# Optimization experiments

Measured on AMD Instinct MI355X. Metric: run time of the kernel, lower is better.

The kernel has to match this reference:

```python
import jax, jax.numpy as jnp
import numpy as np

BETA = 0.25  # commitment_beta from CodebookDecoder default


def setup_inputs() -> dict:
    key = jax.random.key(0)
    k1, k2, k3 = jax.random.split(key, 3)
    Q, B, K, D = 2048, 40000, 2048, 512
    return {
        "query_emb": jax.random.normal(k1, (Q, D), dtype=jnp.float32),
        "entity_emb": jax.random.normal(k2, (B, D), dtype=jnp.float32),
        "codebook": jax.random.normal(k3, (K, D), dtype=jnp.float32),
    }


def _quantize(x, codebook):
    # Nearest-neighbor lookup. torch.norm(x[:,None]-cb[None]) argmin is
    # equivalent to argmin of squared distance, expanded to avoid the
    x2 = jnp.sum(x * x, axis=1, keepdims=True)            # (B, 1)
    c2 = jnp.sum(codebook * codebook, axis=1)             # (K,)
    d2 = x2 - 2.0 * (x @ codebook.T) + c2[None, :]        # (B, K)
    idx = jnp.argmin(d2, axis=1)                          # (B,)
    quant = codebook[idx]                                 # (B, D) gather
    # vq_loss = mse(quant.detach(), x) + beta * mse(quant, x.detach())
    vq_loss = jnp.mean((jax.lax.stop_gradient(quant) - x) ** 2) \
        + BETA * jnp.mean((quant - jax.lax.stop_gradient(x)) ** 2)
    return quant, idx, vq_loss


def reference(query_emb, entity_emb, codebook):
    quant, idx, vq_loss = _quantize(entity_emb, codebook)
    score = query_emb @ quant.T                           # (Q, B)
    return score, vq_loss, idx
```

## Files before the change

### kernel.cpp

```cpp
#include <hip/hip_runtime.h>
#include <stdint.h>

#define Q    2048
#define NB   40000
#define NK   2048
#define ND   512
#define SCORE_SIZE (Q * NB)

#define BM 256
#define BN 256
#define BK 64

typedef __bf16 bf16;
typedef bf16  bf16x8 __attribute__((ext_vector_type(8)));
typedef float f32x4  __attribute__((ext_vector_type(4)));

__device__ __forceinline__ unsigned short f2bf_rne(float f) {
    unsigned int u = __float_as_uint(f);
    u += 0x7FFFu + ((u >> 16) & 1u);
    return (unsigned short)(u >> 16);
}

__device__ __forceinline__ void gl2lds16(const void* g, void* l) {
    __builtin_amdgcn_global_load_lds(
        (const __attribute__((address_space(1))) void*)g,
        (__attribute__((address_space(3))) void*)l, 16, 0, 0);
}

__global__ __launch_bounds__(256) void c2_kernel(const float* __restrict__ cb,
                                                 float* __restrict__ c2) {
    int wave = threadIdx.x >> 6, lane = threadIdx.x & 63;
    int row  = blockIdx.x * 4 + wave;
    const float4* p = (const float4*)(cb + (size_t)row * ND);
    float4 a = p[lane];
    float4 b = p[lane + 64];
    float s = a.x*a.x + a.y*a.y + a.z*a.z + a.w*a.w
            + b.x*b.x + b.y*b.y + b.z*b.z + b.w*b.w;
    #pragma unroll
    for (int off = 32; off; off >>= 1) s += __shfl_down(s, off);
    if (lane == 0) c2[row] = s;
}

__global__ __launch_bounds__(256) void cvt_bf16_kernel(const float* __restrict__ src,
                                                       unsigned short* __restrict__ dst) {
    int i = (blockIdx.x * 256 + threadIdx.x) * 4;
    float4 v = *(const float4*)(src + i);
    uint2 u;
    u.x = (unsigned int)f2bf_rne(v.x) | ((unsigned int)f2bf_rne(v.y) << 16);
    u.y = (unsigned int)f2bf_rne(v.z) | ((unsigned int)f2bf_rne(v.w) << 16);
    *(uint2*)(dst + i) = u;
}

__device__ __forceinline__ void top2_insert(float& v1, int& i1, float& v2, int& i2,
                                            float w, int j) {
    if (w < v1 || (w == v1 && j < i1)) { v2 = v1; i2 = i1; v1 = w; i1 = j; }
    else if (w < v2 || (w == v2 && j < i2)) { v2 = w; i2 = j; }
}

__device__ __forceinline__ void mfma_tile256(const unsigned short* __restrict__ Ab,
                                             const unsigned short* __restrict__ Bb,
                                             f32x4 (&acc)[8][4],
                                             int wm, int wn, int lr, int quad) {
    #pragma unroll
    for (int kq = 0; kq < 2; ++kq) {
        bf16x8 af[8], bfr[4];
        #pragma unroll
        for (int mi = 0; mi < 8; ++mi) {
            int r = wm * 128 + mi * 16 + lr;
            int ch = (kq * 4 + quad) ^ (lr & 7);
            af[mi] = *(const bf16x8*)(Ab + ((size_t)r * 8 + ch) * 8);
        }
        #pragma unroll
        for (int ni = 0; ni < 4; ++ni) {
            int r = wn * 64 + ni * 16 + lr;
            int ch = (kq * 4 + quad) ^ (lr & 7);
            bfr[ni] = *(const bf16x8*)(Bb + ((size_t)r * 8 + ch) * 8);
        }
        #pragma unroll
        for (int mi = 0; mi < 8; ++mi)
            #pragma unroll
            for (int ni = 0; ni < 4; ++ni)
                acc[mi][ni] = __builtin_amdgcn_mfma_f32_16x16x32_bf16(
                    af[mi], bfr[ni], acc[mi][ni], 0, 0, 0);
    }
}

__device__ __forceinline__ void tile_coords8(int bid, int& fast8, int& slow157) {
    int wg = (bid & 7) * 157 + (bid >> 3);
    fast8   = wg & 7;
    slow157 = wg >> 3;
}

template<bool PRE>
__device__ __forceinline__ void stage_dist256(
        const float* __restrict__ entf, const unsigned short* __restrict__ ehi,
        const unsigned short* __restrict__ chi,
        unsigned short* Eb, unsigned short* Cb,
        int b0, int k0, int kt, int tid, int wave) {
    #pragma unroll
    for (int j = 0; j < 4; ++j) {
        int q = j * 512 + tid;
        int r = q >> 3;
        int cs = (q & 7) ^ (r & 7);
        gl2lds16(chi + (size_t)(k0 + r) * ND + kt + cs * 8,
                 Cb + (size_t)(j * 512 + wave * 64) * 8);
        int br = b0 + r; br = br < NB ? br : NB - 1;
        if (PRE) {
            gl2lds16(ehi + (size_t)br * ND + kt + cs * 8,
                     Eb + (size_t)(j * 512 + wave * 64) * 8);
        } else {
            const float* s = entf + (size_t)br * ND + kt + cs * 8;
            float4 a = *(const float4*)s;
            float4 b = *(const float4*)(s + 4);
            uint4 hp;
            hp.x = (unsigned int)f2bf_rne(a.x) | ((unsigned int)f2bf_rne(a.y) << 16);
            hp.y = (unsigned int)f2bf_rne(a.z) | ((unsigned int)f2bf_rne(a.w) << 16);
            hp.z = (unsigned int)f2bf_rne(b.x) | ((unsigned int)f2bf_rne(b.y) << 16);
            hp.w = (unsigned int)f2bf_rne(b.z) | ((unsigned int)f2bf_rne(b.w) << 16);
            *(uint4*)(Eb + (size_t)q * 8) = hp;
        }
    }
}

template<bool PRE>
__global__ __launch_bounds__(512, 2) void dist_mfma_kernel(
        const float* __restrict__ entf, const unsigned short* __restrict__ ehi,
        const unsigned short* __restrict__ chi,
        const float* __restrict__ c2g, float4* __restrict__ partial) {
    __shared__ unsigned short Es[2][BM * BK];
    __shared__ unsigned short Cs[2][BN * BK];
    int tid = threadIdx.x;
    int by, bx;
    tile_coords8(blockIdx.x, by, bx);
    int b0 = bx * BM;
    int k0 = by * BN;
    int lane = tid & 63, wave = tid >> 6;
    int wm = wave >> 2, wn = wave & 3;
    int lr = lane & 15, quad = lane >> 4;

    f32x4 acc[8][4] = {};

    stage_dist256<PRE>(entf, ehi, chi, Es[0], Cs[0], b0, k0, 0, tid, wave);
    __syncthreads();

    for (int t = 0; t < 8; ++t) {
        if (t < 7)
            stage_dist256<PRE>(entf, ehi, chi, Es[(t + 1) & 1], Cs[(t + 1) & 1],
                               b0, k0, (t + 1) * BK, tid, wave);
        mfma_tile256(Es[t & 1], Cs[t & 1], acc, wm, wn, lr, quad);
        __syncthreads();
    }

    float c2v[4];
    #pragma unroll
    for (int ni = 0; ni < 4; ++ni) c2v[ni] = c2g[k0 + wn * 64 + ni * 16 + lr];

    #pragma unroll
    for (int mi = 0; mi < 8; ++mi) {
        #pragma unroll
        for (int rr = 0; rr < 4; ++rr) {
            float v1 = 3.4e38f, v2 = 3.4e38f;
            int i1 = 0x7FFFFFFF, i2 = 0x7FFFFFFF;
            #pragma unroll
            for (int ni = 0; ni < 4; ++ni) {
                float w = c2v[ni] - 2.0f * acc[mi][ni][rr];
                top2_insert(v1, i1, v2, i2, w, k0 + wn * 64 + ni * 16 + lr);
            }
            #pragma unroll
            for (int off = 1; off < 16; off <<= 1) {
                float ov1 = __shfl_xor(v1, off); int oi1 = __shfl_xor(i1, off);
                float ov2 = __shfl_xor(v2, off); int oi2 = __shfl_xor(i2, off);
                top2_insert(v1, i1, v2, i2, ov1, oi1);
                top2_insert(v1, i1, v2, i2, ov2, oi2);
            }
            int b = b0 + wm * 128 + mi * 16 + quad * 4 + rr;
            if (lr == 0 && b < NB)
                partial[(size_t)(by * 4 + wn) * NB + b] =
                    make_float4(v1, __int_as_float(i1), v2, __int_as_float(i2));
        }
    }
}

__global__ __launch_bounds__(256) void cand_merge_kernel(
        const float4* __restrict__ partial, int* __restrict__ cand) {
    int b = blockIdx.x * 256 + threadIdx.x;
    if (b >= NB) return;
    float tv[8]; int ti[8];
    #pragma unroll
    for (int s = 0; s < 8; ++s) { tv[s] = 3.4e38f; ti[s] = 0x7FFFFFFF; }
    for (int g = 0; g < 32; ++g) {
        float4 p = partial[(size_t)g * NB + b];
        float pv[2] = {p.x, p.z};
        int   pi[2] = {__float_as_int(p.y), __float_as_int(p.w)};
        #pragma unroll
        for (int t = 0; t < 2; ++t) {
            float w = pv[t]; int j = pi[t];
            #pragma unroll
            for (int s = 0; s < 8; ++s) {
                if (w < tv[s] || (w == tv[s] && j < ti[s])) {
                    float tmpv = tv[s]; int tmpi = ti[s];
                    tv[s] = w; ti[s] = j; w = tmpv; j = tmpi;
                }
            }
        }
    }
    #pragma unroll
    for (int s = 0; s < 8; ++s) cand[(size_t)b * 8 + s] = ti[s];
}

__global__ __launch_bounds__(512) void rescore_kernel(
        const float* __restrict__ ent, const float* __restrict__ cb,
        const float* __restrict__ c2g, const int* __restrict__ cand,
        unsigned short* __restrict__ quantb, float* __restrict__ out_idx,
        float* __restrict__ acc) {
    int b = blockIdx.x;
    int wave = threadIdx.x >> 6, lane = threadIdx.x & 63;
    int k = cand[(size_t)b * 8 + wave];
    const float4* xp = (const float4*)(ent + (size_t)b * ND);
    const float4* cp = (const float4*)(cb + (size_t)k * ND);
    float4 x0 = xp[lane * 2], x1 = xp[lane * 2 + 1];
    float4 c0 = cp[lane * 2], c1 = cp[lane * 2 + 1];
    float s = x0.x*c0.x + x0.y*c0.y + x0.z*c0.z + x0.w*c0.w
            + x1.x*c1.x + x1.y*c1.y + x1.z*c1.z + x1.w*c1.w;
    #pragma unroll
    for (int off = 32; off; off >>= 1) s += __shfl_down(s, off);
    __shared__ float vws[8];
    __shared__ int   kws[8];
    __shared__ int   win;
    if (lane == 0) { vws[wave] = c2g[k] - 2.0f * s; kws[wave] = k; }
    __syncthreads();
    if (threadIdx.x == 0) {
        float bv = vws[0]; int bk = kws[0], bw = 0;
        #pragma unroll
        for (int w = 1; w < 8; ++w) {
            if (vws[w] < bv || (vws[w] == bv && kws[w] < bk)) {
                bv = vws[w]; bk = kws[w]; bw = w;
            }
        }
        win = bw;
        out_idx[b] = (float)bk;
    }
    __syncthreads();
    if (wave == win) {
        uint4 qp;
        qp.x = (unsigned int)f2bf_rne(c0.x) | ((unsigned int)f2bf_rne(c0.y) << 16);
        qp.y = (unsigned int)f2bf_rne(c0.z) | ((unsigned int)f2bf_rne(c0.w) << 16);
        qp.z = (unsigned int)f2bf_rne(c1.x) | ((unsigned int)f2bf_rne(c1.y) << 16);
        qp.w = (unsigned int)f2bf_rne(c1.z) | ((unsigned int)f2bf_rne(c1.w) << 16);
        *(uint4*)(quantb + (size_t)b * ND + lane * 8) = qp;
        float d0 = c0.x - x0.x, d1 = c0.y - x0.y, d2 = c0.z - x0.z, d3 = c0.w - x0.w;
        float d4 = c1.x - x1.x, d5 = c1.y - x1.y, d6 = c1.z - x1.z, d7 = c1.w - x1.w;
        float l = d0*d0 + d1*d1 + d2*d2 + d3*d3 + d4*d4 + d5*d5 + d6*d6 + d7*d7;
        #pragma unroll
        for (int off = 32; off; off >>= 1) l += __shfl_down(l, off);
        if (lane == 0) atomicAdd(acc, l);
    }
}

__global__ void vq_final_kernel(const float* __restrict__ acc, float* __restrict__ out) {
    out[0] = 1.25f * acc[0] / (float)(NB * ND);
}

__device__ __forceinline__ void stage_score256(
        const unsigned short* __restrict__ Aq, const unsigned short* __restrict__ Bq,
        unsigned short* Ab, unsigned short* Bb,
        int m0, int n0, int kt, int tid, int wave) {
    #pragma unroll
    for (int j = 0; j < 4; ++j) {
        int q = j * 512 + tid;
        int r = q >> 3;
        int cs = (q & 7) ^ (r & 7);
        gl2lds16(Aq + (size_t)(m0 + r) * ND + kt + cs * 8,
                 Ab + (size_t)(j * 512 + wave * 64) * 8);
        int nr = n0 + r; nr = nr < NB ? nr : NB - 1;
        gl2lds16(Bq + (size_t)nr * ND + kt + cs * 8,
                 Bb + (size_t)(j * 512 + wave * 64) * 8);
    }
}

__global__ __launch_bounds__(512, 2) void score_kernel(
        const unsigned short* __restrict__ Aq, const unsigned short* __restrict__ Bq,
        float* __restrict__ C) {
    __shared__ unsigned short As[2][BM * BK];
    __shared__ unsigned short Bs[2][BN * BK];
    int tid = threadIdx.x;
    int bm, bn;
    tile_coords8(blockIdx.x, bm, bn);
    int m0 = bm * BM;
    int n0 = bn * BN;
    int lane = tid & 63, wave = tid >> 6;
    int wm = wave >> 2, wn = wave & 3;
    int lr = lane & 15, quad = lane >> 4;

    f32x4 acc[8][4] = {};

    stage_score256(Aq, Bq, As[0], Bs[0], m0, n0, 0, tid, wave);
    __syncthreads();

    for (int t = 0; t < 8; ++t) {
        if (t < 7)
            stage_score256(Aq, Bq, As[(t + 1) & 1], Bs[(t + 1) & 1],
                           m0, n0, (t + 1) * BK, tid, wave);
        mfma_tile256(As[t & 1], Bs[t & 1], acc, wm, wn, lr, quad);
        __syncthreads();
    }

    #pragma unroll
    for (int mi = 0; mi < 8; ++mi) {
        #pragma unroll
        for (int ni = 0; ni < 4; ++ni) {
            int col = n0 + wn * 64 + ni * 16 + lr;
            if (col < NB) {
                #pragma unroll
                for (int r = 0; r < 4; ++r) {
                    int row = m0 + wm * 128 + mi * 16 + quad * 4 + r;
                    C[(size_t)row * NB + col] = acc[mi][ni][r];
                }
            }
        }
    }
}

extern "C" void kernel_launch(void* const* d_in, const int* in_sizes, int n_in,
                              void* d_out, int out_size, void* d_ws, size_t ws_size,
                              hipStream_t stream) {
    const float* qry = (const float*)d_in[0];
    const float* ent = (const float*)d_in[1];
    const float* cb  = (const float*)d_in[2];
    float* out = (float*)d_out;

    char* ws = (char*)d_ws;
    const bool pre = ws_size >= 100ull * 1024 * 1024;

    float4*         partial = (float4*)(ws);
    unsigned short* quantb  = (unsigned short*)(ws);
    size_t off = 40960000;
    unsigned short* ehi = nullptr;
    if (pre) { ehi = (unsigned short*)(ws + off); off += 40960000; }
    unsigned short* chi = (unsigned short*)(ws + off); off += 2097152;
    unsigned short* qb  = (unsigned short*)(ws + off); off += 2097152;
    int*            cand= (int*)(ws + off);            off += 1280000;
    float*          c2  = (float*)(ws + off);          off += 8192;
    float*          acc = (float*)(ws + off);          off += 4;

    hipMemsetAsync(acc, 0, sizeof(float), stream);

    c2_kernel<<<NK / 4, 256, 0, stream>>>(cb, c2);
    cvt_bf16_kernel<<<NK * ND / 1024, 256, 0, stream>>>(cb, chi);
    cvt_bf16_kernel<<<Q * ND / 1024, 256, 0, stream>>>(qry, qb);
    if (pre) {
        cvt_bf16_kernel<<<NB * ND / 1024, 256, 0, stream>>>(ent, ehi);
        dist_mfma_kernel<true><<<1256, 512, 0, stream>>>(
            ent, ehi, chi, c2, partial);
    } else {
        dist_mfma_kernel<false><<<1256, 512, 0, stream>>>(
            ent, nullptr, chi, c2, partial);
    }
    cand_merge_kernel<<<(NB + 255) / 256, 256, 0, stream>>>(partial, cand);
    rescore_kernel<<<NB, 512, 0, stream>>>(ent, cb, c2, cand, quantb,
                                           out + SCORE_SIZE + 1, acc);
    vq_final_kernel<<<1, 1, 0, stream>>>(acc, out + SCORE_SIZE);
    score_kernel<<<1256, 512, 0, stream>>>(qb, quantb, out);
}
```

Measured before the change: 1.937 ms.

## Prefetch two K-tiles ahead with explicit vmcnt waits in GEMM loops

Replaces the load-then-syncthreads double-buffer loop in the score and bf16 distance GEMMs with a pipeline that issues the first two tiles up front. Each iteration waits on vmcnt only for the older tile's async global-to-LDS loads, then refills the just-consumed buffer with the tile two steps ahead. The aim is to keep more memory traffic in flight and hide load latency behind the MFMA work. The loop is fully unrolled and now relies on hand-placed waitcnt and barrier instructions, which risks races if the outstanding-load count assumption (8 per stage) is wrong.

```diff
diff --git a/kernel.cpp b/kernel.cpp
--- a/kernel.cpp
+++ b/kernel.cpp
@@ -91,10 +91,26 @@
     slow157 = wg >> 3;
 }
 
-template<bool PRE>
-__device__ __forceinline__ void stage_dist256(
-        const float* __restrict__ entf, const unsigned short* __restrict__ ehi,
-        const unsigned short* __restrict__ chi,
+__device__ __forceinline__ void stage2(
+        const unsigned short* __restrict__ P0, int a0, int lim0,
+        const unsigned short* __restrict__ P1, int b0, int lim1,
+        unsigned short* B0, unsigned short* B1, int kt, int tid, int wave) {
+    #pragma unroll
+    for (int j = 0; j < 4; ++j) {
+        int q = j * 512 + tid;
+        int r = q >> 3;
+        int cs = (q & 7) ^ (r & 7);
+        int ra = a0 + r; ra = ra < lim0 ? ra : lim0 - 1;
+        int rb = b0 + r; rb = rb < lim1 ? rb : lim1 - 1;
+        gl2lds16(P0 + (size_t)ra * ND + kt + cs * 8,
+                 B0 + (size_t)(j * 512 + wave * 64) * 8);
+        gl2lds16(P1 + (size_t)rb * ND + kt + cs * 8,
+                 B1 + (size_t)(j * 512 + wave * 64) * 8);
+    }
+}
+
+__device__ __forceinline__ void stage_dist_f32(
+        const float* __restrict__ entf, const unsigned short* __restrict__ chi,
         unsigned short* Eb, unsigned short* Cb,
         int b0, int k0, int kt, int tid, int wave) {
     #pragma unroll
@@ -105,22 +121,33 @@
         gl2lds16(chi + (size_t)(k0 + r) * ND + kt + cs * 8,
                  Cb + (size_t)(j * 512 + wave * 64) * 8);
         int br = b0 + r; br = br < NB ? br : NB - 1;
-        if (PRE) {
-            gl2lds16(ehi + (size_t)br * ND + kt + cs * 8,
-                     Eb + (size_t)(j * 512 + wave * 64) * 8);
-        } else {
-            const float* s = entf + (size_t)br * ND + kt + cs * 8;
-            float4 a = *(const float4*)s;
-            float4 b = *(const float4*)(s + 4);
-            uint4 hp;
-            hp.x = (unsigned int)f2bf_rne(a.x) | ((unsigned int)f2bf_rne(a.y) << 16);
-            hp.y = (unsigned int)f2bf_rne(a.z) | ((unsigned int)f2bf_rne(a.w) << 16);
-            hp.z = (unsigned int)f2bf_rne(b.x) | ((unsigned int)f2bf_rne(b.y) << 16);
-            hp.w = (unsigned int)f2bf_rne(b.z) | ((unsigned int)f2bf_rne(b.w) << 16);
-            *(uint4*)(Eb + (size_t)q * 8) = hp;
-        }
-    }
-}
+        const float* s = entf + (size_t)br * ND + kt + cs * 8;
+        float4 a = *(const float4*)s;
+        float4 b = *(const float4*)(s + 4);
+        uint4 hp;
+        hp.x = (unsigned int)f2bf_rne(a.x) | ((unsigned int)f2bf_rne(a.y) << 16);
+        hp.y = (unsigned int)f2bf_rne(a.z) | ((unsigned int)f2bf_rne(a.w) << 16);
+        hp.z = (unsigned int)f2bf_rne(b.x) | ((unsigned int)f2bf_rne(b.y) << 16);
+        hp.w = (unsigned int)f2bf_rne(b.z) | ((unsigned int)f2bf_rne(b.w) << 16);
+        *(uint4*)(Eb + (size_t)q * 8) = hp;
+    }
+}
+
+#define PIPE_KLOOP(STAGE_T2, COMPUTE_T)                                        \
+    _Pragma("unroll")                                                          \
+    for (int t = 0; t < 8; ++t) {                                              \
+        if (t < 7) asm volatile("s_waitcnt vmcnt(8)" ::: "memory");            \
+        else       asm volatile("s_waitcnt vmcnt(0)" ::: "memory");            \
+        __builtin_amdgcn_sched_barrier(0);                                     \
+        __builtin_amdgcn_s_barrier();          \
+        __builtin_amdgcn_sched_barrier(0);                                     \
+        COMPUTE_T;                                                             \
+        asm volatile("s_waitcnt lgkmcnt(0)" ::: "memory");                     \
+        __builtin_amdgcn_sched_barrier(0);                                     \
+        __builtin_amdgcn_s_barrier();          \
+        __builtin_amdgcn_sched_barrier(0);                                     \
+        if (t < 6) { STAGE_T2; }               \
+    }
 
 template<bool PRE>
 __global__ __launch_bounds__(512, 2) void dist_mfma_kernel(
@@ -140,15 +167,23 @@
 
     f32x4 acc[8][4] = {};
 
-    stage_dist256<PRE>(entf, ehi, chi, Es[0], Cs[0], b0, k0, 0, tid, wave);
-    __syncthreads();
-
-    for (int t = 0; t < 8; ++t) {
-        if (t < 7)
-            stage_dist256<PRE>(entf, ehi, chi, Es[(t + 1) & 1], Cs[(t + 1) & 1],
+    if constexpr (PRE) {
+        stage2(ehi, b0, NB, chi, k0, NK, Es[0], Cs[0], 0,  tid, wave);
+        stage2(ehi, b0, NB, chi, k0, NK, Es[1], Cs[1], BK, tid, wave);
+        PIPE_KLOOP(
+            stage2(ehi, b0, NB, chi, k0, NK, Es[t & 1], Cs[t & 1],
+                   (t + 2) * BK, tid, wave),
+            mfma_tile256(Es[t & 1], Cs[t & 1], acc, wm, wn, lr, quad));
+    } else {
+        stage_dist_f32(entf, chi, Es[0], Cs[0], b0, k0, 0, tid, wave);
+        __syncthreads();
+        for (int t = 0; t < 8; ++t) {
+            if (t < 7)
+                stage_dist_f32(entf, chi, Es[(t + 1) & 1], Cs[(t + 1) & 1],
                                b0, k0, (t + 1) * BK, tid, wave);
-        mfma_tile256(Es[t & 1], Cs[t & 1], acc, wm, wn, lr, quad);
-        __syncthreads();
+            mfma_tile256(Es[t & 1], Cs[t & 1], acc, wm, wn, lr, quad);
+            __syncthreads();
+        }
     }
 
     float c2v[4];
@@ -261,23 +296,6 @@
     out[0] = 1.25f * acc[0] / (float)(NB * ND);
 }
 
-__device__ __forceinline__ void stage_score256(
-        const unsigned short* __restrict__ Aq, const unsigned short* __restrict__ Bq,
-        unsigned short* Ab, unsigned short* Bb,
-        int m0, int n0, int kt, int tid, int wave) {
-    #pragma unroll
-    for (int j = 0; j < 4; ++j) {
-        int q = j * 512 + tid;
-        int r = q >> 3;
-        int cs = (q & 7) ^ (r & 7);
-        gl2lds16(Aq + (size_t)(m0 + r) * ND + kt + cs * 8,
-                 Ab + (size_t)(j * 512 + wave * 64) * 8);
-        int nr = n0 + r; nr = nr < NB ? nr : NB - 1;
-        gl2lds16(Bq + (size_t)nr * ND + kt + cs * 8,
-                 Bb + (size_t)(j * 512 + wave * 64) * 8);
-    }
-}
-
 __global__ __launch_bounds__(512, 2) void score_kernel(
         const unsigned short* __restrict__ Aq, const unsigned short* __restrict__ Bq,
         float* __restrict__ C) {
@@ -294,16 +312,12 @@
 
     f32x4 acc[8][4] = {};
 
-    stage_score256(Aq, Bq, As[0], Bs[0], m0, n0, 0, tid, wave);
-    __syncthreads();
-
-    for (int t = 0; t < 8; ++t) {
-        if (t < 7)
-            stage_score256(Aq, Bq, As[(t + 1) & 1], Bs[(t + 1) & 1],
-                           m0, n0, (t + 1) * BK, tid, wave);
-        mfma_tile256(As[t & 1], Bs[t & 1], acc, wm, wn, lr, quad);
-        __syncthreads();
-    }
+    stage2(Aq, m0, Q, Bq, n0, NB, As[0], Bs[0], 0,  tid, wave);
+    stage2(Aq, m0, Q, Bq, n0, NB, As[1], Bs[1], BK, tid, wave);
+    PIPE_KLOOP(
+        stage2(Aq, m0, Q, Bq, n0, NB, As[t & 1], Bs[t & 1],
+               (t + 2) * BK, tid, wave),
+        mfma_tile256(As[t & 1], Bs[t & 1], acc, wm, wn, lr, quad));
 
     #pragma unroll
     for (int mi = 0; mi < 8; ++mi) {
```

New measurement: 1.920 ms. About the same (-0.9%).
